# Kernel optimization log

Hardware: AMD Instinct MI355X
Metric: run time of the kernel (lower is better)

The kernel has to match this reference:

```python
import jax, jax.numpy as jnp
import numpy as np

B, T, DIM, DIM_EPS, H = 4, 1024, 2048, 2048, 16
HD = DIM // H        # 128, value head dim
HDE = DIM_EPS // H   # 128, q/k head dim


def setup_inputs() -> dict:
    key = jax.random.key(0)
    ks = jax.random.split(key, 6)
    s = 0.02
    # rotary frequencies as in llama-style precompute (theta=10000)
    inv_freq = 1.0 / (10000.0 ** (np.arange(0, HDE, 2, dtype=np.float32) / HDE))
    t = np.arange(T, dtype=np.float32)
    ang = np.outer(t, inv_freq)  # (T, HDE//2)
    return {
        "v": jax.random.normal(ks[0], (B, T, DIM), jnp.float32),
        "x_eps": jax.random.normal(ks[1], (B, T, DIM_EPS), jnp.float32),
        "freqs_cos": jnp.asarray(np.cos(ang)),
        "freqs_sin": jnp.asarray(np.sin(ang)),
        "W_eps_attn": jax.random.normal(ks[2], (DIM_EPS, 2 * DIM_EPS), jnp.float32) * s,
        "W_attn": jax.random.normal(ks[3], (DIM, DIM), jnp.float32) * s,
        "W_proj": jax.random.normal(ks[4], (DIM, DIM), jnp.float32) * s,
        "W_eps_proj": jax.random.normal(ks[5], (DIM_EPS, DIM_EPS), jnp.float32) * s,
    }


def _rope(x, cos, sin):
    # x: (B, T, H, HDE) -> complex-multiply by freqs_cis of shape (T, HDE//2)
    xr = x.reshape(*x.shape[:-1], -1, 2)
    x_re, x_im = xr[..., 0], xr[..., 1]
    c = cos[None, :, None, :]  # (1, T, 1, HDE//2)
    s = sin[None, :, None, :]
    o_re = x_re * c - x_im * s
    o_im = x_re * s + x_im * c
    return jnp.stack([o_re, o_im], axis=-1).reshape(x.shape)


def reference(v, x_eps, freqs_cos, freqs_sin, W_eps_attn, W_attn, W_proj, W_eps_proj):
    Bn, Tn, C = v.shape
    qk = x_eps @ W_eps_attn            # (B, T, 2*DIM_EPS)
    q, k = jnp.split(qk, 2, axis=-1)
    vp = v @ W_attn                    # (B, T, DIM)
    q = _rope(q.reshape(Bn, Tn, H, HDE), freqs_cos, freqs_sin)
    k = _rope(k.reshape(Bn, Tn, H, HDE), freqs_cos, freqs_sin)
    q = q.transpose(0, 2, 1, 3)        # (B, H, T, HDE)
    k = k.transpose(0, 2, 1, 3)
    vh = vp.reshape(Bn, Tn, H, HD).transpose(0, 2, 1, 3)
    scale = 1.0 / jnp.sqrt(jnp.asarray(HDE, q.dtype))
    scores = jnp.einsum("bhqd,bhkd->bhqk", q, k) * scale
    causal = jnp.tril(jnp.ones((Tn, Tn), bool))
    scores = jnp.where(causal[None, None], scores, jnp.finfo(scores.dtype).min)
    att = jax.nn.softmax(scores, axis=-1)
    y = jnp.einsum("bhqk,bhkd->bhqd", att, vh)
    y = y.transpose(0, 2, 1, 3).reshape(Bn, Tn, C)
    v_out = y @ W_proj
    x_eps_out = x_eps @ W_eps_proj
    return (v_out, x_eps_out)
```

## Files before the change

### kernel.cpp

```cpp
#include <hip/hip_runtime.h>
#include <stdint.h>

typedef __attribute__((ext_vector_type(8))) short  short8;
typedef __attribute__((ext_vector_type(4))) float  f32x4;
typedef __attribute__((ext_vector_type(4))) float  float4v;
typedef __attribute__((ext_vector_type(4))) unsigned short ushort4v;

#define DEV __device__ __forceinline__

DEV unsigned short f2bf(float f) {
    union { float f; unsigned int u; } x; x.f = f;
    unsigned int u = x.u;
    unsigned int r = (u + 0x7fffu + ((u >> 16) & 1u)) >> 16;
    return (unsigned short)r;
}
DEV float bf2f(unsigned short b) {
    union { unsigned int u; float f; } x; x.u = ((unsigned int)b) << 16;
    return x.f;
}

DEV void gll16(const void* g, void* l) {
    __builtin_amdgcn_global_load_lds(
        (const __attribute__((address_space(1))) void*)g,
        (__attribute__((address_space(3))) void*)l, 16, 0, 0);
}

#define MROWS 4096
#define KDIM  2048
#define NQK   4096

__global__ void cast_f32_bf16(const float* __restrict__ in,
                              unsigned short* __restrict__ out, int n4) {
    int i = blockIdx.x * blockDim.x + threadIdx.x;
    if (i < n4) {
        float4v f = ((const float4v*)in)[i];
        ushort4v o;
        o[0] = f2bf(f[0]); o[1] = f2bf(f[1]); o[2] = f2bf(f[2]); o[3] = f2bf(f[3]);
        ((ushort4v*)out)[i] = o;
    }
}

__global__ void transpose_cast(const float* __restrict__ W,
                               unsigned short* __restrict__ Wt, int K, int N) {
    __shared__ float tile[32][33];
    int tx = threadIdx.x, ty = threadIdx.y;
    int n0 = blockIdx.x * 32, k0 = blockIdx.y * 32;
#pragma unroll
    for (int j = 0; j < 32; j += 8)
        tile[ty + j][tx] = W[(size_t)(k0 + ty + j) * N + n0 + tx];
    __syncthreads();
#pragma unroll
    for (int j = 0; j < 32; j += 8)
        Wt[(size_t)(n0 + ty + j) * K + k0 + tx] = f2bf(tile[tx][ty + j]);
}

__global__ void transpose_v(const unsigned short* __restrict__ vp,
                            unsigned short* __restrict__ vpT) {
    __shared__ unsigned short tile[32][34];
    int tx = threadIdx.x, ty = threadIdx.y;
    int R0 = blockIdx.y * 32;
    int c0 = blockIdx.x * 32;
    int bh = R0 >> 7, d0 = R0 & 127;
    int b = bh >> 4, h = bh & 15;
#pragma unroll
    for (int j = 0; j < 32; j += 8)
        tile[ty + j][tx] = vp[(size_t)(b * 1024 + c0 + ty + j) * 2048 + h * 128 + d0 + tx];
    __syncthreads();
#pragma unroll
    for (int j = 0; j < 32; j += 8)
        vpT[(size_t)(R0 + ty + j) * 1024 + c0 + tx] = tile[tx][ty + j];
}

__global__ __launch_bounds__(512, 2) void gemm256(
    const unsigned short* __restrict__ A0g, const unsigned short* __restrict__ B0g,
    float* __restrict__ Cf0, unsigned short* __restrict__ Ch0,
    int N0, int tx0, int nb0, int outbf0,
    const unsigned short* __restrict__ A1g, const unsigned short* __restrict__ B1g,
    float* __restrict__ Cf1, unsigned short* __restrict__ Ch1,
    int N1, int tx1, int outbf1, int K) {

    __shared__ __align__(16) char lds[131072];

    int blk = blockIdx.x;
    const unsigned short* Ag; const unsigned short* Bg;
    float* Cf; unsigned short* Ch; int N, tx, outbf, nwg;
    if (blk < nb0) { Ag = A0g; Bg = B0g; Cf = Cf0; Ch = Ch0; N = N0; tx = tx0; outbf = outbf0; nwg = nb0; }
    else { blk -= nb0; Ag = A1g; Bg = B1g; Cf = Cf1; Ch = Ch1; N = N1; tx = tx1; outbf = outbf1; nwg = gridDim.x - nb0; }
    { int cpx = nwg >> 3; blk = (blk & 7) * cpx + (blk >> 3); }
    const int bx = blk % tx, by = blk / tx;

    const int tid = threadIdx.x;
    const int lane = tid & 63;
    const int w  = tid >> 6;
    const int lr = lane & 15, lk = lane >> 4;
    const int wm = w >> 2, wn = w & 3;
    const int cswz16 = (lk ^ ((lr >> 3) << 1)) * 16;
    const int rdOff  = lr * 64 + cswz16;
    const int bRow0B = (wn & 1) * 4096;

    const unsigned short* Arow = Ag + (size_t)(by * 256) * K;
    const unsigned short* Brow = Bg + (size_t)(bx * 256) * K;

    const int srow = tid >> 2;
    const int sclog = (tid & 3) ^ (((tid >> 5) & 1) << 1);
    const unsigned short* aSt0 = Arow + (size_t)srow * K + sclog * 8;
    const unsigned short* aSt1 = aSt0 + (size_t)128 * K;
    const unsigned short* bSt0 = Brow + (size_t)srow * K + sclog * 8;
    const unsigned short* bSt1 = bSt0 + (size_t)128 * K;

    char* sA0 = lds;            char* sB0 = lds + 32768;
    char* sA1 = lds + 65536;    char* sB1 = lds + 98304;
    const int sOff = tid * 16;

    const char* aB0 = lds + wm * 16384;
    const char* aB1 = aB0 + 65536;
    const char* bB0 = lds + 32768 + (wn >> 1) * 16384;
    const char* bB1 = bB0 + 65536;

    f32x4 acc[8][4];
#pragma unroll
    for (int m = 0; m < 8; ++m)
#pragma unroll
        for (int n = 0; n < 4; ++n) acc[m][n] = (f32x4){0.f, 0.f, 0.f, 0.f};

    const int NT = K >> 6;

    auto STAGE = [&](const unsigned short* srcHalf, int k0, char* ldsHalf) {
        gll16(srcHalf + k0,      ldsHalf + sOff);
        gll16(srcHalf + k0 + 32, ldsHalf + 8192 + sOff);
    };

    STAGE(aSt0, 0, sA0);  STAGE(aSt1, 0, sA0 + 16384);
    STAGE(bSt0, 0, sB0);  STAGE(bSt1, 0, sB0 + 16384);
    STAGE(aSt0, 64, sA1);
    asm volatile("s_waitcnt vmcnt(2)" ::: "memory");
    __builtin_amdgcn_s_barrier();

#define MFMA_BF(a, b, c) __builtin_amdgcn_mfma_f32_16x16x32_bf16(a, b, c, 0, 0, 0)

#define RD_A(BASE, MH)                                                              \
    _Pragma("unroll") for (int i = 0; i < 4; ++i) {                                 \
        Ar[i][0] = *(const short8*)((BASE) +        (MH) * 4096 + i * 1024 + rdOff); \
        Ar[i][1] = *(const short8*)((BASE) + 8192 + (MH) * 4096 + i * 1024 + rdOff); \
    }

#define RD_B(BASE, NH)                                                                        \
    _Pragma("unroll") for (int j = 0; j < 2; ++j) {                                           \
        Br[j][0] = *(const short8*)((BASE) +        bRow0B + ((NH) * 2 + j) * 1024 + rdOff);  \
        Br[j][1] = *(const short8*)((BASE) + 8192 + bRow0B + ((NH) * 2 + j) * 1024 + rdOff);  \
    }

#define MFMA16(MH, NH)                                                       \
    __builtin_amdgcn_s_setprio(1);                                           \
    _Pragma("unroll") for (int ks = 0; ks < 2; ++ks)                         \
        _Pragma("unroll") for (int i = 0; i < 4; ++i)                        \
            _Pragma("unroll") for (int j = 0; j < 2; ++j)                    \
                acc[(MH) * 4 + i][(NH) * 2 + j] =                            \
                    MFMA_BF(Ar[i][ks], Br[j][ks], acc[(MH) * 4 + i][(NH) * 2 + j]); \
    __builtin_amdgcn_s_setprio(0);

#define PH(RDS, STG, MFMAQ, VMW)                               \
    {                                                          \
        RDS;                                                   \
        STG;                                                   \
        __builtin_amdgcn_s_barrier();                          \
        asm volatile("s_waitcnt lgkmcnt(0)" ::: "memory");     \
        __builtin_amdgcn_sched_barrier(0);                     \
        MFMAQ;                                                 \
        VMW;                                                   \
        __builtin_amdgcn_s_barrier();                          \
    }

#define VMC2 asm volatile("s_waitcnt vmcnt(2)" ::: "memory")

    short8 Ar[4][2], Br[2][2];

    for (int i2 = 0; i2 < NT; i2 += 2) {
        const int kt1 = (i2 + 1) * 64;
        const int kA  = (i2 + 2 < NT ? i2 + 2 : NT - 1) * 64;
        const int kA3 = (i2 + 3 < NT ? i2 + 3 : NT - 1) * 64;

        PH({ RD_A(aB0, 0) RD_B(bB0, 0) },
           { STAGE(aSt1, kt1, sA1 + 16384); STAGE(bSt0, kt1, sB1); STAGE(bSt1, kt1, sB1 + 16384); },
           MFMA16(0, 0), {})
        PH({ RD_B(bB0, 1) }, {}, MFMA16(0, 1), {})
        PH({ RD_A(aB0, 1) RD_B(bB0, 0) }, {}, MFMA16(1, 0), {})
        PH({ RD_B(bB0, 1) },
           { STAGE(aSt0, kA, sA0); },
           MFMA16(1, 1), VMC2)

        PH({ RD_A(aB1, 0) RD_B(bB1, 0) },
           { STAGE(aSt1, kA, sA0 + 16384); STAGE(bSt0, kA, sB0); STAGE(bSt1, kA, sB0 + 16384); },
           MFMA16(0, 0), {})
        PH({ RD_B(bB1, 1) }, {}, MFMA16(0, 1), {})
        PH({ RD_A(aB1, 1) RD_B(bB1, 0) }, {}, MFMA16(1, 0), {})
        PH({ RD_B(bB1, 1) },
           { STAGE(aSt0, kA3, sA1); },
           MFMA16(1, 1), VMC2)
    }
    asm volatile("s_waitcnt vmcnt(0)" ::: "memory");
#undef RD_A
#undef RD_B
#undef MFMA16
#undef PH
#undef VMC2

    if (outbf) {
#pragma unroll
        for (int mf = 0; mf < 8; ++mf)
#pragma unroll
            for (int nf = 0; nf < 4; ++nf)
#pragma unroll
                for (int r = 0; r < 4; ++r) {
                    int row = by * 256 + wm * 128 + mf * 16 + lk * 4 + r;
                    int col = bx * 256 + wn * 64 + nf * 16 + lr;
                    Ch[(size_t)row * N + col] = f2bf(acc[mf][nf][r]);
                }
    } else {
#pragma unroll
        for (int mf = 0; mf < 8; ++mf)
#pragma unroll
            for (int nf = 0; nf < 4; ++nf)
#pragma unroll
                for (int r = 0; r < 4; ++r) {
                    int row = by * 256 + wm * 128 + mf * 16 + lk * 4 + r;
                    int col = bx * 256 + wn * 64 + nf * 16 + lr;
                    Cf[(size_t)row * N + col] = acc[mf][nf][r];
                }
    }
}

__global__ void rope_kernel(unsigned short* __restrict__ qk,
                            const float* __restrict__ fcos,
                            const float* __restrict__ fsin) {
    int idx  = blockIdx.x * 256 + threadIdx.x;
    int row  = idx >> 9;
    int g    = idx & 511;
    int t    = row & 1023;
    int half = g >> 8;
    int hp   = g & 255;
    int h    = hp >> 4;
    int ig   = hp & 15;
    int col  = half * 2048 + h * 128 + ig * 8;
    size_t off = (size_t)row * 4096 + col;

    short8 v = *(short8*)(qk + off);
    int i0 = ig * 4;
    float4v c = *(const float4v*)(fcos + t * 64 + i0);
    float4v s = *(const float4v*)(fsin + t * 64 + i0);
    short8 o;
#pragma unroll
    for (int p = 0; p < 4; ++p) {
        float re = bf2f((unsigned short)v[2 * p]);
        float im = bf2f((unsigned short)v[2 * p + 1]);
        o[2 * p]     = (short)f2bf(re * c[p] - im * s[p]);
        o[2 * p + 1] = (short)f2bf(re * s[p] + im * c[p]);
    }
    *(short8*)(qk + off) = o;
}

__global__ __launch_bounds__(256) void attn_kernel(
    const unsigned short* __restrict__ qk,
    const unsigned short* __restrict__ vpT,
    unsigned short* __restrict__ y) {

    const int bh = blockIdx.x;
    const int qt = 7 - (int)blockIdx.y;
    const int b = bh >> 4, h = bh & 15;
    const int qb0 = qt * 128;

    __shared__ __align__(16) unsigned short Kt[64 * 128];
    __shared__ __align__(16) unsigned short Vt[128 * 64];
    __shared__ __align__(16) unsigned short Pl[4 * 32 * 72];

    const int tid = threadIdx.x, w = tid >> 6, lane = tid & 63;
    const int lr = lane & 15, lk = lane >> 4;

    const unsigned short* Qb = qk + (size_t)(b * 1024) * 4096 + h * 128;
    const unsigned short* Kb = Qb + 2048;
    const unsigned short* Vg = vpT + (size_t)bh * 128 * 1024;
    unsigned short* Pw = &Pl[w * 32 * 72];

    short8 qf[2][4];
#pragma unroll
    for (int m = 0; m < 2; ++m) {
        const unsigned short* qrow = Qb + (size_t)(qb0 + w * 32 + m * 16 + lr) * 4096;
#pragma unroll
        for (int db = 0; db < 4; ++db)
            qf[m][db] = *(const short8*)(qrow + db * 32 + lk * 8);
    }

    f32x4 acc[2][8];
#pragma unroll
    for (int m = 0; m < 2; ++m)
#pragma unroll
        for (int n = 0; n < 8; ++n) acc[m][n] = (f32x4){0.f, 0.f, 0.f, 0.f};
    float m_i[2][4], l_i[2][4];
#pragma unroll
    for (int m = 0; m < 2; ++m)
#pragma unroll
        for (int r = 0; r < 4; ++r) { m_i[m][r] = -1e30f; l_i[m][r] = 0.f; }

    const int nkt = 2 * qt + 2;
    for (int kt = 0; kt < nkt; ++kt) {
#pragma unroll
        for (int c = 0; c < 4; ++c) {
            int base = w * 4096 + c * 1024;
            int row  = (base >> 8) + (lane >> 4);
            int colB = (lane & 15) * 16;
            int scol = colB ^ ((row & 7) << 4);
            gll16(Kb + (size_t)(kt * 64 + row) * 4096 + (scol >> 1),
                  (char*)Kt + base);
        }
#pragma unroll
        for (int c = 0; c < 4; ++c) {
            int base = w * 4096 + c * 1024;
            int d    = (base >> 7) + (lane >> 3);
            int colB = (lane & 7) * 16;
            int scol = colB ^ ((d & 7) << 4);
            gll16(Vg + (size_t)d * 1024 + kt * 64 + (scol >> 1),
                  (char*)Vt + base);
        }
        __syncthreads();

        f32x4 s[2][4];
#pragma unroll
        for (int m = 0; m < 2; ++m)
#pragma unroll
            for (int n = 0; n < 4; ++n) s[m][n] = (f32x4){0.f, 0.f, 0.f, 0.f};
#pragma unroll
        for (int db = 0; db < 4; ++db)
#pragma unroll
            for (int n = 0; n < 4; ++n) {
                int krow = n * 16 + lr;
                int cb = (db * 64 + lk * 16) ^ ((krow & 7) << 4);
                short8 kf = *(const short8*)((const char*)Kt + krow * 256 + cb);
                s[0][n] = __builtin_amdgcn_mfma_f32_16x16x32_bf16(qf[0][db], kf, s[0][n], 0, 0, 0);
                s[1][n] = __builtin_amdgcn_mfma_f32_16x16x32_bf16(qf[1][db], kf, s[1][n], 0, 0, 0);
            }

        const float sc = 0.08838834764831845f;
        const bool diag = (kt >= 2 * qt);
#pragma unroll
        for (int m = 0; m < 2; ++m)
#pragma unroll
            for (int n = 0; n < 4; ++n)
#pragma unroll
                for (int r = 0; r < 4; ++r) {
                    float v = s[m][n][r] * sc;
                    if (diag) {
                        int q   = qb0 + w * 32 + m * 16 + lk * 4 + r;
                        int key = kt * 64 + n * 16 + lr;
                        if (key > q) v = -1e30f;
                    }
                    s[m][n][r] = v;
                }

#pragma unroll
        for (int m = 0; m < 2; ++m) {
            float pm[4];
#pragma unroll
            for (int r = 0; r < 4; ++r)
                pm[r] = fmaxf(fmaxf(s[m][0][r], s[m][1][r]), fmaxf(s[m][2][r], s[m][3][r]));
#pragma unroll
            for (int o = 1; o < 16; o <<= 1)
#pragma unroll
                for (int r = 0; r < 4; ++r)
                    pm[r] = fmaxf(pm[r], __shfl_xor(pm[r], o, 16));

            float resc[4], rs[4];
#pragma unroll
            for (int r = 0; r < 4; ++r) {
                float mn = fmaxf(m_i[m][r], pm[r]);
                resc[r] = __expf(m_i[m][r] - mn);
                m_i[m][r] = mn;
                rs[r] = 0.f;
            }
#pragma unroll
            for (int n = 0; n < 4; ++n)
#pragma unroll
                for (int r = 0; r < 4; ++r) {
                    float p = __expf(s[m][n][r] - m_i[m][r]);
                    s[m][n][r] = p;
                    rs[r] += p;
                }
#pragma unroll
            for (int o = 1; o < 16; o <<= 1)
#pragma unroll
                for (int r = 0; r < 4; ++r)
                    rs[r] += __shfl_xor(rs[r], o, 16);
#pragma unroll
            for (int r = 0; r < 4; ++r)
                l_i[m][r] = l_i[m][r] * resc[r] + rs[r];
#pragma unroll
            for (int n = 0; n < 8; ++n)
#pragma unroll
                for (int r = 0; r < 4; ++r)
                    acc[m][n][r] *= resc[r];

#pragma unroll
            for (int n = 0; n < 4; ++n)
#pragma unroll
                for (int r = 0; r < 4; ++r)
                    Pw[(m * 16 + lk * 4 + r) * 72 + n * 16 + lr] = f2bf(s[m][n][r]);
        }

#pragma unroll
        for (int ks = 0; ks < 2; ++ks) {
            short8 pf0 = *(const short8*)&Pw[(lr) * 72 + ks * 32 + lk * 8];
            short8 pf1 = *(const short8*)&Pw[(16 + lr) * 72 + ks * 32 + lk * 8];
#pragma unroll
            for (int n8 = 0; n8 < 8; ++n8) {
                int d  = n8 * 16 + lr;
                int cb = (ks * 64 + lk * 16) ^ ((d & 7) << 4);
                short8 vf = *(const short8*)((const char*)Vt + d * 128 + cb);
                acc[0][n8] = __builtin_amdgcn_mfma_f32_16x16x32_bf16(pf0, vf, acc[0][n8], 0, 0, 0);
                acc[1][n8] = __builtin_amdgcn_mfma_f32_16x16x32_bf16(pf1, vf, acc[1][n8], 0, 0, 0);
            }
        }
        __syncthreads();
    }

    unsigned short* yb = y + (size_t)(b * 1024) * 2048 + h * 128;
#pragma unroll
    for (int m = 0; m < 2; ++m)
#pragma unroll
        for (int n8 = 0; n8 < 8; ++n8)
#pragma unroll
            for (int r = 0; r < 4; ++r) {
                int t = qb0 + w * 32 + m * 16 + lk * 4 + r;
                int d = n8 * 16 + lr;
                yb[(size_t)t * 2048 + d] = f2bf(acc[m][n8][r] / l_i[m][r]);
            }
}

extern "C" void kernel_launch(void* const* d_in, const int* in_sizes, int n_in,
                              void* d_out, int out_size, void* d_ws, size_t ws_size,
                              hipStream_t stream) {
    const float* v_in  = (const float*)d_in[0];
    const float* xeps  = (const float*)d_in[1];
    const float* fcos  = (const float*)d_in[2];
    const float* fsin  = (const float*)d_in[3];
    const float* Wea   = (const float*)d_in[4];
    const float* Wa    = (const float*)d_in[5];
    const float* Wp    = (const float*)d_in[6];
    const float* Wep   = (const float*)d_in[7];
    float* out = (float*)d_out;

    char* ws = (char*)d_ws;
    unsigned short* xe16 = (unsigned short*)ws;  ws += (size_t)MROWS * KDIM * 2;
    unsigned short* v16  = (unsigned short*)ws;  ws += (size_t)MROWS * KDIM * 2;
    unsigned short* WeaT = (unsigned short*)ws;  ws += (size_t)NQK * KDIM * 2;
    unsigned short* WaT  = (unsigned short*)ws;  ws += (size_t)KDIM * KDIM * 2;
    unsigned short* WpT  = (unsigned short*)ws;  ws += (size_t)KDIM * KDIM * 2;
    unsigned short* WepT = (unsigned short*)ws;  ws += (size_t)KDIM * KDIM * 2;
    unsigned short* qk16 = (unsigned short*)ws;  ws += (size_t)MROWS * NQK * 2;
    unsigned short* vp16 = (unsigned short*)ws;  ws += (size_t)MROWS * KDIM * 2;
    unsigned short* y16  = (unsigned short*)ws;  ws += (size_t)MROWS * KDIM * 2;
    unsigned short* vpT  = v16;

    cast_f32_bf16<<<8192, 256, 0, stream>>>(xeps, xe16, MROWS * KDIM / 4);
    cast_f32_bf16<<<8192, 256, 0, stream>>>(v_in, v16,  MROWS * KDIM / 4);

    transpose_cast<<<dim3(NQK / 32, KDIM / 32), dim3(32, 8), 0, stream>>>(Wea, WeaT, KDIM, NQK);
    transpose_cast<<<dim3(KDIM / 32, KDIM / 32), dim3(32, 8), 0, stream>>>(Wa,  WaT,  KDIM, KDIM);
    transpose_cast<<<dim3(KDIM / 32, KDIM / 32), dim3(32, 8), 0, stream>>>(Wp,  WpT,  KDIM, KDIM);
    transpose_cast<<<dim3(KDIM / 32, KDIM / 32), dim3(32, 8), 0, stream>>>(Wep, WepT, KDIM, KDIM);

    gemm256<<<256, 512, 0, stream>>>(
        xe16, WeaT, nullptr, qk16, NQK, 16, 256, 1,
        xe16, WeaT, nullptr, qk16, NQK, 16, 1, KDIM);

    rope_kernel<<<8192, 256, 0, stream>>>(qk16, fcos, fsin);

    gemm256<<<256, 512, 0, stream>>>(
        v16,  WaT,  nullptr, vp16, KDIM, 8, 128, 1,
        xe16, WepT, out + (size_t)MROWS * KDIM, nullptr, KDIM, 8, 0, KDIM);

    transpose_v<<<dim3(1024 / 32, 8192 / 32), dim3(32, 8), 0, stream>>>(vp16, vpT);

    attn_kernel<<<dim3(64, 8), 256, 0, stream>>>(qk16, vpT, y16);

    gemm256<<<128, 512, 0, stream>>>(
        y16, WpT, out, nullptr, KDIM, 8, 128, 0,
        y16, WpT, out, nullptr, KDIM, 8, 0, KDIM);
}
```

Before: 329.4 us.

## Fuse prep kernels and RoPE into GEMM, split-K output proj, register-prefetch attention tiles

```diff
diff --git a/kernel.cpp b/kernel.cpp
--- a/kernel.cpp
+++ b/kernel.cpp
@@ -5,6 +5,7 @@
 typedef __attribute__((ext_vector_type(4))) float  f32x4;
 typedef __attribute__((ext_vector_type(4))) float  float4v;
 typedef __attribute__((ext_vector_type(4))) unsigned short ushort4v;
+typedef __attribute__((ext_vector_type(4))) unsigned int   u32x4;
 
 #define DEV __device__ __forceinline__
 
@@ -29,22 +30,35 @@
 #define KDIM  2048
 #define NQK   4096
 
-__global__ void cast_f32_bf16(const float* __restrict__ in,
-                              unsigned short* __restrict__ out, int n4) {
-    int i = blockIdx.x * blockDim.x + threadIdx.x;
-    if (i < n4) {
+__global__ void prep_kernel(
+    const float* __restrict__ xeps, const float* __restrict__ v_in,
+    const float* __restrict__ Wea, const float* __restrict__ Wa,
+    const float* __restrict__ Wp,  const float* __restrict__ Wep,
+    unsigned short* __restrict__ xe16, unsigned short* __restrict__ v16,
+    unsigned short* __restrict__ WeaT, unsigned short* __restrict__ WaT,
+    unsigned short* __restrict__ WpT,  unsigned short* __restrict__ WepT) {
+
+    __shared__ float tile[32][33];
+    const int blk = blockIdx.x, tid = threadIdx.x;
+
+    if (blk < 16384) {
+        const float* in = (blk < 8192) ? xeps : v_in;
+        unsigned short* out = (blk < 8192) ? xe16 : v16;
+        int i = (blk & 8191) * 256 + tid;
         float4v f = ((const float4v*)in)[i];
         ushort4v o;
         o[0] = f2bf(f[0]); o[1] = f2bf(f[1]); o[2] = f2bf(f[2]); o[3] = f2bf(f[3]);
         ((ushort4v*)out)[i] = o;
-    }
-}
-
-__global__ void transpose_cast(const float* __restrict__ W,
-                               unsigned short* __restrict__ Wt, int K, int N) {
-    __shared__ float tile[32][33];
-    int tx = threadIdx.x, ty = threadIdx.y;
-    int n0 = blockIdx.x * 32, k0 = blockIdx.y * 32;
+        return;
+    }
+    const float* W; unsigned short* Wt; int K, N, local;
+    if (blk < 24576)      { W = Wea; Wt = WeaT; K = KDIM; N = NQK;  local = blk - 16384; }
+    else if (blk < 28672) { W = Wa;  Wt = WaT;  K = KDIM; N = KDIM; local = blk - 24576; }
+    else if (blk < 32768) { W = Wp;  Wt = WpT;  K = KDIM; N = KDIM; local = blk - 28672; }
+    else                  { W = Wep; Wt = WepT; K = KDIM; N = KDIM; local = blk - 32768; }
+    const int ntiles = N >> 5;
+    const int n0 = (local % ntiles) * 32, k0 = (local / ntiles) * 32;
+    const int tx = tid & 31, ty = tid >> 5;
 #pragma unroll
     for (int j = 0; j < 32; j += 8)
         tile[ty + j][tx] = W[(size_t)(k0 + ty + j) * N + n0 + tx];
@@ -52,6 +66,16 @@
 #pragma unroll
     for (int j = 0; j < 32; j += 8)
         Wt[(size_t)(n0 + ty + j) * K + k0 + tx] = f2bf(tile[tx][ty + j]);
+}
+
+__global__ void add_f32(float* __restrict__ out, const float* __restrict__ add, int n4) {
+    int i = blockIdx.x * blockDim.x + threadIdx.x;
+    if (i < n4) {
+        float4v a = ((const float4v*)out)[i];
+        float4v b = ((const float4v*)add)[i];
+        a[0] += b[0]; a[1] += b[1]; a[2] += b[2]; a[3] += b[3];
+        ((float4v*)out)[i] = a;
+    }
 }
 
 __global__ void transpose_v(const unsigned short* __restrict__ vp,
@@ -77,15 +101,17 @@
     int N0, int tx0, int nb0, int outbf0,
     const unsigned short* __restrict__ A1g, const unsigned short* __restrict__ B1g,
     float* __restrict__ Cf1, unsigned short* __restrict__ Ch1,
-    int N1, int tx1, int outbf1, int K) {
+    int N1, int tx1, int outbf1, int Kst, int Kl,
+    const float* __restrict__ rC, const float* __restrict__ rS,
+    int rope0, int rope1) {
 
     __shared__ __align__(16) char lds[131072];
 
     int blk = blockIdx.x;
     const unsigned short* Ag; const unsigned short* Bg;
-    float* Cf; unsigned short* Ch; int N, tx, outbf, nwg;
-    if (blk < nb0) { Ag = A0g; Bg = B0g; Cf = Cf0; Ch = Ch0; N = N0; tx = tx0; outbf = outbf0; nwg = nb0; }
-    else { blk -= nb0; Ag = A1g; Bg = B1g; Cf = Cf1; Ch = Ch1; N = N1; tx = tx1; outbf = outbf1; nwg = gridDim.x - nb0; }
+    float* Cf; unsigned short* Ch; int N, tx, outbf, nwg, ropeF;
+    if (blk < nb0) { Ag = A0g; Bg = B0g; Cf = Cf0; Ch = Ch0; N = N0; tx = tx0; outbf = outbf0; nwg = nb0; ropeF = rope0; }
+    else { blk -= nb0; Ag = A1g; Bg = B1g; Cf = Cf1; Ch = Ch1; N = N1; tx = tx1; outbf = outbf1; nwg = gridDim.x - nb0; ropeF = rope1; }
     { int cpx = nwg >> 3; blk = (blk & 7) * cpx + (blk >> 3); }
     const int bx = blk % tx, by = blk / tx;
 
@@ -98,15 +124,15 @@
     const int rdOff  = lr * 64 + cswz16;
     const int bRow0B = (wn & 1) * 4096;
 
-    const unsigned short* Arow = Ag + (size_t)(by * 256) * K;
-    const unsigned short* Brow = Bg + (size_t)(bx * 256) * K;
+    const unsigned short* Arow = Ag + (size_t)(by * 256) * Kst;
+    const unsigned short* Brow = Bg + (size_t)(bx * 256) * Kst;
 
     const int srow = tid >> 2;
     const int sclog = (tid & 3) ^ (((tid >> 5) & 1) << 1);
-    const unsigned short* aSt0 = Arow + (size_t)srow * K + sclog * 8;
-    const unsigned short* aSt1 = aSt0 + (size_t)128 * K;
-    const unsigned short* bSt0 = Brow + (size_t)srow * K + sclog * 8;
-    const unsigned short* bSt1 = bSt0 + (size_t)128 * K;
+    const unsigned short* aSt0 = Arow + (size_t)srow * Kst + sclog * 8;
+    const unsigned short* aSt1 = aSt0 + (size_t)128 * Kst;
+    const unsigned short* bSt0 = Brow + (size_t)srow * Kst + sclog * 8;
+    const unsigned short* bSt1 = bSt0 + (size_t)128 * Kst;
 
     char* sA0 = lds;            char* sB0 = lds + 32768;
     char* sA1 = lds + 65536;    char* sB1 = lds + 98304;
@@ -123,7 +149,7 @@
 #pragma unroll
         for (int n = 0; n < 4; ++n) acc[m][n] = (f32x4){0.f, 0.f, 0.f, 0.f};
 
-    const int NT = K >> 6;
+    const int NT = Kl >> 6;
 
     auto STAGE = [&](const unsigned short* srcHalf, int k0, char* ldsHalf) {
         gll16(srcHalf + k0,      ldsHalf + sOff);
@@ -138,8 +164,8 @@
 
 #define MFMA_BF(a, b, c) __builtin_amdgcn_mfma_f32_16x16x32_bf16(a, b, c, 0, 0, 0)
 
-#define RD_A(BASE, MH)                                                              \
-    _Pragma("unroll") for (int i = 0; i < 4; ++i) {                                 \
+#define RD_A(BASE, MH)                                                               \
+    _Pragma("unroll") for (int i = 0; i < 4; ++i) {                                  \
         Ar[i][0] = *(const short8*)((BASE) +        (MH) * 4096 + i * 1024 + rdOff); \
         Ar[i][1] = *(const short8*)((BASE) + 8192 + (MH) * 4096 + i * 1024 + rdOff); \
     }
@@ -206,16 +232,37 @@
 #undef VMC2
 
     if (outbf) {
-#pragma unroll
-        for (int mf = 0; mf < 8; ++mf)
-#pragma unroll
-            for (int nf = 0; nf < 4; ++nf)
-#pragma unroll
-                for (int r = 0; r < 4; ++r) {
-                    int row = by * 256 + wm * 128 + mf * 16 + lk * 4 + r;
-                    int col = bx * 256 + wn * 64 + nf * 16 + lr;
-                    Ch[(size_t)row * N + col] = f2bf(acc[mf][nf][r]);
-                }
+        if (ropeF) {
+#pragma unroll
+            for (int mf = 0; mf < 8; ++mf)
+#pragma unroll
+                for (int nf = 0; nf < 4; ++nf)
+#pragma unroll
+                    for (int r = 0; r < 4; ++r) {
+                        int row = by * 256 + wm * 128 + mf * 16 + lk * 4 + r;
+                        int col = bx * 256 + wn * 64 + nf * 16 + lr;
+                        float val = acc[mf][nf][r];
+                        float part = __shfl_xor(val, 1);
+                        int t = row & 1023;
+                        int i = (col & 127) >> 1;
+                        float c = rC[t * 64 + i];
+                        float s = rS[t * 64 + i];
+                        float o = (lr & 1) ? (part * s + val * c)
+                                           : (val * c - part * s);
+                        Ch[(size_t)row * N + col] = f2bf(o);
+                    }
+        } else {
+#pragma unroll
+            for (int mf = 0; mf < 8; ++mf)
+#pragma unroll
+                for (int nf = 0; nf < 4; ++nf)
+#pragma unroll
+                    for (int r = 0; r < 4; ++r) {
+                        int row = by * 256 + wm * 128 + mf * 16 + lk * 4 + r;
+                        int col = bx * 256 + wn * 64 + nf * 16 + lr;
+                        Ch[(size_t)row * N + col] = f2bf(acc[mf][nf][r]);
+                    }
+        }
     } else {
 #pragma unroll
         for (int mf = 0; mf < 8; ++mf)
@@ -230,35 +277,6 @@
     }
 }
 
-__global__ void rope_kernel(unsigned short* __restrict__ qk,
-                            const float* __restrict__ fcos,
-                            const float* __restrict__ fsin) {
-    int idx  = blockIdx.x * 256 + threadIdx.x;
-    int row  = idx >> 9;
-    int g    = idx & 511;
-    int t    = row & 1023;
-    int half = g >> 8;
-    int hp   = g & 255;
-    int h    = hp >> 4;
-    int ig   = hp & 15;
-    int col  = half * 2048 + h * 128 + ig * 8;
-    size_t off = (size_t)row * 4096 + col;
-
-    short8 v = *(short8*)(qk + off);
-    int i0 = ig * 4;
-    float4v c = *(const float4v*)(fcos + t * 64 + i0);
-    float4v s = *(const float4v*)(fsin + t * 64 + i0);
-    short8 o;
-#pragma unroll
-    for (int p = 0; p < 4; ++p) {
-        float re = bf2f((unsigned short)v[2 * p]);
-        float im = bf2f((unsigned short)v[2 * p + 1]);
-        o[2 * p]     = (short)f2bf(re * c[p] - im * s[p]);
-        o[2 * p + 1] = (short)f2bf(re * s[p] + im * c[p]);
-    }
-    *(short8*)(qk + off) = o;
-}
-
 __global__ __launch_bounds__(256) void attn_kernel(
     const unsigned short* __restrict__ qk,
     const unsigned short* __restrict__ vpT,
@@ -281,6 +299,7 @@
     const unsigned short* Vg = vpT + (size_t)bh * 128 * 1024;
     unsigned short* Pw = &Pl[w * 32 * 72];
 
+
     short8 qf[2][4];
 #pragma unroll
     for (int m = 0; m < 2; ++m) {
@@ -302,26 +321,36 @@
         for (int r = 0; r < 4; ++r) { m_i[m][r] = -1e30f; l_i[m][r] = 0.f; }
 
     const int nkt = 2 * qt + 2;
+
+#pragma unroll
+    for (int c = 0; c < 4; ++c) {
+        int base = w * 4096 + c * 1024;
+        int row  = (base >> 8) + (lane >> 4);
+        int scol = ((lane & 15) * 16) ^ ((row & 7) << 4);
+        gll16(Kb + (size_t)row * 4096 + (scol >> 1), (char*)Kt + base);
+        int d    = (base >> 7) + (lane >> 3);
+        int svol = ((lane & 7) * 16) ^ ((d & 7) << 4);
+        gll16(Vg + (size_t)d * 1024 + (svol >> 1), (char*)Vt + base);
+    }
+    __syncthreads();
+
+    u32x4 kreg[4], vreg[4];
+
     for (int kt = 0; kt < nkt; ++kt) {
-#pragma unroll
-        for (int c = 0; c < 4; ++c) {
-            int base = w * 4096 + c * 1024;
-            int row  = (base >> 8) + (lane >> 4);
-            int colB = (lane & 15) * 16;
-            int scol = colB ^ ((row & 7) << 4);
-            gll16(Kb + (size_t)(kt * 64 + row) * 4096 + (scol >> 1),
-                  (char*)Kt + base);
+        const bool pf = (kt + 1 < nkt);
+        if (pf) {
+            const int ktn = kt + 1;
+#pragma unroll
+            for (int c = 0; c < 4; ++c) {
+                int base = w * 4096 + c * 1024;
+                int row  = (base >> 8) + (lane >> 4);
+                int scol = ((lane & 15) * 16) ^ ((row & 7) << 4);
+                kreg[c] = *(const u32x4*)(Kb + (size_t)(ktn * 64 + row) * 4096 + (scol >> 1));
+                int d    = (base >> 7) + (lane >> 3);
+                int svol = ((lane & 7) * 16) ^ ((d & 7) << 4);
+                vreg[c] = *(const u32x4*)(Vg + (size_t)d * 1024 + ktn * 64 + (svol >> 1));
+            }
         }
-#pragma unroll
-        for (int c = 0; c < 4; ++c) {
-            int base = w * 4096 + c * 1024;
-            int d    = (base >> 7) + (lane >> 3);
-            int colB = (lane & 7) * 16;
-            int scol = colB ^ ((d & 7) << 4);
-            gll16(Vg + (size_t)d * 1024 + kt * 64 + (scol >> 1),
-                  (char*)Vt + base);
-        }
-        __syncthreads();
 
         f32x4 s[2][4];
 #pragma unroll
@@ -368,14 +397,27 @@
                 for (int r = 0; r < 4; ++r)
                     pm[r] = fmaxf(pm[r], __shfl_xor(pm[r], o, 16));
 
-            float resc[4], rs[4];
-#pragma unroll
-            for (int r = 0; r < 4; ++r) {
-                float mn = fmaxf(m_i[m][r], pm[r]);
-                resc[r] = __expf(m_i[m][r] - mn);
-                m_i[m][r] = mn;
-                rs[r] = 0.f;
+            bool small = true;
+#pragma unroll
+            for (int r = 0; r < 4; ++r)
+                small = small && (pm[r] <= m_i[m][r] + 8.0f);
+            if (!__all((int)small)) {
+                float resc[4];
+#pragma unroll
+                for (int r = 0; r < 4; ++r) {
+                    float mn = fmaxf(m_i[m][r], pm[r]);
+                    resc[r] = __expf(m_i[m][r] - mn);
+                    m_i[m][r] = mn;
+                    l_i[m][r] *= resc[r];
+                }
+#pragma unroll
+                for (int n = 0; n < 8; ++n)
+#pragma unroll
+                    for (int r = 0; r < 4; ++r)
+                        acc[m][n][r] *= resc[r];
             }
+
+            float rs[4] = {0.f, 0.f, 0.f, 0.f};
 #pragma unroll
             for (int n = 0; n < 4; ++n)
 #pragma unroll
@@ -391,12 +433,7 @@
                     rs[r] += __shfl_xor(rs[r], o, 16);
 #pragma unroll
             for (int r = 0; r < 4; ++r)
-                l_i[m][r] = l_i[m][r] * resc[r] + rs[r];
-#pragma unroll
-            for (int n = 0; n < 8; ++n)
-#pragma unroll
-                for (int r = 0; r < 4; ++r)
-                    acc[m][n][r] *= resc[r];
+                l_i[m][r] += rs[r];
 
 #pragma unroll
             for (int n = 0; n < 4; ++n)
@@ -416,6 +453,16 @@
                 short8 vf = *(const short8*)((const char*)Vt + d * 128 + cb);
                 acc[0][n8] = __builtin_amdgcn_mfma_f32_16x16x32_bf16(pf0, vf, acc[0][n8], 0, 0, 0);
                 acc[1][n8] = __builtin_amdgcn_mfma_f32_16x16x32_bf16(pf1, vf, acc[1][n8], 0, 0, 0);
+            }
+        }
+        __syncthreads();
+
+        if (pf) {
+#pragma unroll
+            for (int c = 0; c < 4; ++c) {
+                int base = w * 4096 + c * 1024;
+                *(u32x4*)((char*)Kt + base + lane * 16) = kreg[c];
+                *(u32x4*)((char*)Vt + base + lane * 16) = vreg[c];
             }
         }
         __syncthreads();
@@ -458,30 +505,29 @@
     unsigned short* vp16 = (unsigned short*)ws;  ws += (size_t)MROWS * KDIM * 2;
     unsigned short* y16  = (unsigned short*)ws;  ws += (size_t)MROWS * KDIM * 2;
     unsigned short* vpT  = v16;
-
-    cast_f32_bf16<<<8192, 256, 0, stream>>>(xeps, xe16, MROWS * KDIM / 4);
-    cast_f32_bf16<<<8192, 256, 0, stream>>>(v_in, v16,  MROWS * KDIM / 4);
-
-    transpose_cast<<<dim3(NQK / 32, KDIM / 32), dim3(32, 8), 0, stream>>>(Wea, WeaT, KDIM, NQK);
-    transpose_cast<<<dim3(KDIM / 32, KDIM / 32), dim3(32, 8), 0, stream>>>(Wa,  WaT,  KDIM, KDIM);
-    transpose_cast<<<dim3(KDIM / 32, KDIM / 32), dim3(32, 8), 0, stream>>>(Wp,  WpT,  KDIM, KDIM);
-    transpose_cast<<<dim3(KDIM / 32, KDIM / 32), dim3(32, 8), 0, stream>>>(Wep, WepT, KDIM, KDIM);
+    float* projP = (float*)qk16;
+
+    prep_kernel<<<36864, 256, 0, stream>>>(xeps, v_in, Wea, Wa, Wp, Wep,
+                                           xe16, v16, WeaT, WaT, WpT, WepT);
 
     gemm256<<<256, 512, 0, stream>>>(
         xe16, WeaT, nullptr, qk16, NQK, 16, 256, 1,
-        xe16, WeaT, nullptr, qk16, NQK, 16, 1, KDIM);
-
-    rope_kernel<<<8192, 256, 0, stream>>>(qk16, fcos, fsin);
+        xe16, WeaT, nullptr, qk16, NQK, 16, 1, KDIM, KDIM,
+        fcos, fsin, 1, 1);
 
     gemm256<<<256, 512, 0, stream>>>(
         v16,  WaT,  nullptr, vp16, KDIM, 8, 128, 1,
-        xe16, WepT, out + (size_t)MROWS * KDIM, nullptr, KDIM, 8, 0, KDIM);
+        xe16, WepT, out + (size_t)MROWS * KDIM, nullptr, KDIM, 8, 0, KDIM, KDIM,
+        fcos, fsin, 0, 0);
 
     transpose_v<<<dim3(1024 / 32, 8192 / 32), dim3(32, 8), 0, stream>>>(vp16, vpT);
 
     attn_kernel<<<dim3(64, 8), 256, 0, stream>>>(qk16, vpT, y16);
 
-    gemm256<<<128, 512, 0, stream>>>(
-        y16, WpT, out, nullptr, KDIM, 8, 128, 0,
-        y16, WpT, out, nullptr, KDIM, 8, 0, KDIM);
-}
+    gemm256<<<256, 512, 0, stream>>>(
+        y16,        WpT,        out,   nullptr, KDIM, 8, 128, 0,
+        y16 + 1024, WpT + 1024, projP, nullptr, KDIM, 8, 0, KDIM, 1024,
+        fcos, fsin, 0, 0);
+
+    add_f32<<<8192, 256, 0, stream>>>(out, projP, MROWS * KDIM / 4);
+}
```

Measured after the change: 306.3 us. 1.08x faster.
